# Performance work log

Hardware: AMD Instinct MI355X
Metric: run time of the kernel (lower is better)

The kernel has to match this reference:

```python
import jax, jax.numpy as jnp
import numpy as np

B, D, H, O, E = 16384, 1024, 512, 256, 8


def setup_inputs() -> dict:
    key = jax.random.key(0)
    ks = jax.random.split(key, 8)
    s = lambda k, shape, fan: (jax.random.normal(k, shape, jnp.float32) / np.sqrt(fan).astype(np.float32))
    z = lambda shape: jnp.zeros(shape, jnp.float32)
    return {
        "x": jax.random.normal(ks[0], (B, D), jnp.float32),
        # gating network: D -> 256 -> 128 -> E
        "gw1": s(ks[1], (D, 256), D), "gb1": z((256,)),
        "gw2": s(ks[2], (256, 128), 256), "gb2": z((128,)),
        "gw3": s(ks[3], (128, E), 128), "gb3": z((E,)),
        # experts, batched over expert dim E: D -> H -> H -> O
        "ew1": s(ks[4], (E, D, H), D), "eb1": z((E, H)),
        "ew2": s(ks[5], (E, H, H), H), "eb2": z((E, H)),
        "ew3": s(ks[6], (E, H, O), H), "eb3": z((E, O)),
    }


def reference(x, gw1, gb1, gw2, gb2, gw3, gb3, ew1, eb1, ew2, eb2, ew3, eb3):
    # Gating network (dropout is identity in eval mode)
    g = jax.nn.relu(x @ gw1 + gb1)
    g = jax.nn.relu(g @ gw2 + gb2)
    gates = jax.nn.softmax(g @ gw3 + gb3, axis=1)  # [B, E]
    # All experts run on every token: batched small MLPs over expert axis e
    h = jax.nn.relu(jnp.einsum('bd,edh->ebh', x, ew1) + eb1[:, None, :])   # [E, B, H]
    h = jax.nn.relu(jnp.einsum('ebh,ehk->ebk', h, ew2) + eb2[:, None, :])  # [E, B, H]
    eo = jnp.einsum('ebh,eho->ebo', h, ew3) + eb3[:, None, :]              # [E, B, O]
    # gate-weighted sum over experts
    out = jnp.einsum('ebo,be->bo', eo, gates)  # [B, O]
    return out
```

## Files before the change

kernel.cpp:

```cpp
#include <hip/hip_runtime.h>
#include <hip/hip_bf16.h>

typedef __hip_bfloat16 bf16;
typedef __attribute__((ext_vector_type(8))) __bf16 bf16x8;
typedef __attribute__((ext_vector_type(4))) float f32x4;

#define B_ 16384
#define D_ 1024
#define H_ 512
#define O_ 256
#define E_ 8
#define BC_ 8192
#define NG_ (E_ * H_ + 256)

static_assert(B_ % BC_ == 0, "chunking");

#define GLDS(src, dst) __builtin_amdgcn_global_load_lds( \
    (const __attribute__((address_space(1))) void*)(src), \
    (__attribute__((address_space(3))) void*)(dst), 16, 0, 0)

#define BAR()   asm volatile("s_barrier" ::: "memory")
#define LGKM0() do { asm volatile("s_waitcnt lgkmcnt(0)" ::: "memory"); \
                     __builtin_amdgcn_sched_barrier(0); } while (0)

__global__ void detect_k(const unsigned short* __restrict__ x, int* __restrict__ flag) {
    __shared__ int s;
    if (threadIdx.x == 0) s = 0;
    __syncthreads();
    int big = 0;
    for (int i = threadIdx.x; i < 2048; i += 256)
        if (((x[i] >> 7) & 0xFF) >= 150) big = 1;
    if (big) atomicOr(&s, 1);
    __syncthreads();
    if (threadIdx.x == 0) *flag = s;
}

__global__ void preproc_k(const void* x, bf16* xc,
                          const void* gb1, const void* gb2, const void* gw3,
                          const void* gb3, const void* eb1, const void* eb2,
                          const void* eb3,
                          bf16* gb1c, bf16* gb2c, bf16* gw3c, bf16* gb3c,
                          bf16* eb1c, bf16* eb2c, bf16* eb3c,
                          const void* gw1, const void* gw2,
                          const void* ew1, const void* ew2, const void* ew3,
                          bf16* gw1t, bf16* gw2t,
                          bf16* ew1t, bf16* ew2t, bf16* ew3t,
                          long ew3_zout, long ew3_cstride,
                          const int* __restrict__ flag) {
    const int f = *flag;
    const int tid = threadIdx.y * 32 + threadIdx.x;
    int lin = blockIdx.x;

    if (lin < 1024) {
        const long n8 = (long)B_ * D_ / 8;
        long i = (long)lin * 256 + tid;
        const long stride = 1024 * 256;
        if (f) {
            const float4* s = (const float4*)x;
            for (; i < n8; i += stride) {
                float4 a = s[2 * i], b = s[2 * i + 1];
                bf16 tmp[8];
                tmp[0] = __float2bfloat16(a.x); tmp[1] = __float2bfloat16(a.y);
                tmp[2] = __float2bfloat16(a.z); tmp[3] = __float2bfloat16(a.w);
                tmp[4] = __float2bfloat16(b.x); tmp[5] = __float2bfloat16(b.y);
                tmp[6] = __float2bfloat16(b.z); tmp[7] = __float2bfloat16(b.w);
                *(uint4*)(xc + i * 8) = *(const uint4*)tmp;
            }
        } else {
            const uint4* s = (const uint4*)x;
            for (; i < n8; i += stride) *(uint4*)(xc + i * 8) = s[i];
        }
        return;
    }
    if (lin < 1031) {
        const int id = lin - 1024;
        const void* sp[7] = {gb1, gb2, gw3, gb3, eb1, eb2, eb3};
        bf16* dp[7] = {gb1c, gb2c, gw3c, gb3c, eb1c, eb2c, eb3c};
        const int len[7] = {256, 128, 1024, 8, E_ * H_, E_ * H_, E_ * O_};
        const float* sf = (const float*)sp[id];
        const bf16*  sb = (const bf16*)sp[id];
        bf16* d = dp[id];
        for (int i = tid; i < len[id]; i += 256)
            d[i] = f ? __float2bfloat16(sf[i]) : sb[i];
        return;
    }
    lin -= 1031;
    __shared__ bf16 t[32][33];
    const void* src; bf16* dst; int R, C, bx, by, bz; long z_out, c_stride;
    if (lin < 256) {
        src = gw1; dst = gw1t; R = 1024; C = 256; z_out = 0; c_stride = 1024;
        bx = lin & 7; by = lin >> 3; bz = 0;
    } else if (lin < 288) {
        lin -= 256;
        src = gw2; dst = gw2t; R = 256; C = 128; z_out = 0; c_stride = 256;
        bx = lin & 3; by = lin >> 2; bz = 0;
    } else if (lin < 4384) {
        lin -= 288;
        src = ew1; dst = ew1t; R = 1024; C = 512;
        z_out = (long)H_ * D_; c_stride = D_;
        bx = lin & 15; by = (lin >> 4) & 31; bz = lin >> 9;
    } else if (lin < 6432) {
        lin -= 4384;
        src = ew2; dst = ew2t; R = 512; C = 512;
        z_out = (long)H_ * H_; c_stride = H_;
        bx = lin & 15; by = (lin >> 4) & 15; bz = lin >> 8;
    } else {
        lin -= 6432;
        src = ew3; dst = ew3t; R = 512; C = 256;
        z_out = ew3_zout; c_stride = ew3_cstride;
        bx = lin & 7; by = (lin >> 3) & 15; bz = lin >> 7;
    }
    const long zi = (long)bz * R * C;
    const int xg = bx * 32 + threadIdx.x;
    const int y0 = by * 32;
    const float* inf = (const float*)src;
    const bf16* inb = (const bf16*)src;
#pragma unroll
    for (int i = 0; i < 4; i++) {
        int r = y0 + threadIdx.y + i * 8;
        long idx = zi + (long)r * C + xg;
        t[threadIdx.y + i * 8][threadIdx.x] =
            f ? __float2bfloat16(inf[idx]) : inb[idx];
    }
    __syncthreads();
    const int xr = by * 32 + threadIdx.x;
    const long zo = (long)bz * z_out;
#pragma unroll
    for (int i = 0; i < 4; i++) {
        int c = bx * 32 + threadIdx.y + i * 8;
        dst[zo + (long)c * c_stride + xr] = t[threadIdx.x][threadIdx.y + i * 8];
    }
}

__global__ void gate3_softmax_k(const bf16* __restrict__ g2,
                                const bf16* __restrict__ gw3,
                                const bf16* __restrict__ gb3,
                                float* __restrict__ gates) {
    __shared__ float w[128 * 8];
    __shared__ float bsh[8];
    const int tid = threadIdx.x;
    for (int i = tid; i < 1024; i += 256) w[i] = __bfloat162float(gw3[i]);
    if (tid < 8) bsh[tid] = __bfloat162float(gb3[tid]);
    __syncthreads();

    const long row = (long)blockIdx.x * 256 + tid;
    float acc[8];
#pragma unroll
    for (int o = 0; o < 8; o++) acc[o] = bsh[o];

    const bf16x8* rp8 = (const bf16x8*)(g2 + row * 128);
#pragma unroll 4
    for (int c8 = 0; c8 < 16; c8++) {
        bf16x8 v8 = rp8[c8];
#pragma unroll
        for (int jj = 0; jj < 8; jj++) {
            float v = (float)v8[jj];
            int k = c8 * 8 + jj;
#pragma unroll
            for (int o = 0; o < 8; o++) acc[o] += v * w[k * 8 + o];
        }
    }
    float m = acc[0];
#pragma unroll
    for (int o = 1; o < 8; o++) m = fmaxf(m, acc[o]);
    float s = 0.f;
#pragma unroll
    for (int o = 0; o < 8; o++) { acc[o] = __expf(acc[o] - m); s += acc[o]; }
    const float inv = 1.f / s;
#pragma unroll
    for (int o = 0; o < 8; o++) gates[row * 8 + o] = acc[o] * inv;
}

template <int MODE>
__global__ __launch_bounds__(256, 4)
void gemm_bt(const bf16* __restrict__ A, const bf16* __restrict__ Bt,
             const bf16* __restrict__ bias, const float* __restrict__ gates,
             void* __restrict__ Cout, const bf16* __restrict__ eb3,
             int lda, int ldb, int ldo, int K,
             long a_z, long b_z, long bias_z, long out_z,
             int e_gate, int k_per_e, long a_e, long b_e, long row0) {
    __shared__ __attribute__((aligned(16))) bf16 As[128 * 32];
    __shared__ __attribute__((aligned(16))) bf16 Bs[128 * 32];

    const int tid  = threadIdx.x;
    const int lane = tid & 63;
    const int quad = lane >> 4;
    const int l15  = lane & 15;
    const int wid  = tid >> 6;
    const int wr   = (wid >> 1) << 6;
    const int wc   = (wid & 1) << 6;
    const int z    = blockIdx.z;
    const long m0  = (long)blockIdx.y << 7;
    const long n0  = (long)blockIdx.x << 7;

    const bf16* Az = A + (long)z * a_z;
    const bf16* Bz = Bt + (long)z * b_z;

    f32x4 acc[4][4];
#pragma unroll
    for (int i = 0; i < 4; i++)
#pragma unroll
        for (int j = 0; j < 4; j++) acc[i][j] = (f32x4){0.f, 0.f, 0.f, 0.f};

    const int erow = tid >> 2;
    const int ecol = (tid & 3) << 3;

    const int n_e   = k_per_e ? (K / k_per_e) : 1;
    const int inner = (k_per_e ? k_per_e : K) >> 5;

    for (int e = 0; e < n_e; e++) {
        const bf16* Ae = Az + (long)e * a_e;
        const bf16* Be = Bz + (long)e * b_e;
        for (int kti = 0; kti < inner; kti++) {
            const int kk = kti << 5;
#pragma unroll
            for (int i = 0; i < 2; i++) {
                const int r = (i << 6) + erow;
                GLDS(Ae + (m0 + r) * lda + (kk + ecol), As + r * 32 + ecol);
            }
#pragma unroll
            for (int i = 0; i < 2; i++) {
                const int r = (i << 6) + erow;
                GLDS(Be + (n0 + r) * ldb + (kk + ecol), Bs + r * 32 + ecol);
            }
            __syncthreads();
            bf16x8 af[4], bfr[4];
#pragma unroll
            for (int i = 0; i < 4; i++)
                af[i] = *(const bf16x8*)(As + (wr + i * 16 + l15) * 32 + (quad << 3));
#pragma unroll
            for (int j = 0; j < 4; j++)
                bfr[j] = *(const bf16x8*)(Bs + (wc + j * 16 + l15) * 32 + (quad << 3));
#pragma unroll
            for (int i = 0; i < 4; i++)
#pragma unroll
                for (int j = 0; j < 4; j++)
                    acc[i][j] = __builtin_amdgcn_mfma_f32_16x16x32_bf16(
                        af[i], bfr[j], acc[i][j], 0, 0, 0);
            __syncthreads();
        }
    }

    const int eg = (e_gate >= 0) ? e_gate : z;

    if constexpr (MODE == 0 || MODE == 1) {
        bf16* C = (bf16*)Cout + (long)z * out_z;
        const bf16* bb = bias + (long)z * bias_z;
        float gv[4][4];
        if constexpr (MODE == 1) {
#pragma unroll
            for (int i = 0; i < 4; i++)
#pragma unroll
                for (int rg = 0; rg < 4; rg++)
                    gv[i][rg] = gates[(row0 + m0 + wr + i * 16 + quad * 4 + rg) * 8 + eg];
        }
#pragma unroll
        for (int j = 0; j < 4; j++) {
            const int c = (int)n0 + wc + j * 16 + l15;
            const float bv = __bfloat162float(bb[c]);
#pragma unroll
            for (int i = 0; i < 4; i++) {
#pragma unroll
                for (int rg = 0; rg < 4; rg++) {
                    const long r = m0 + wr + i * 16 + quad * 4 + rg;
                    float v = fmaxf(acc[i][j][rg] + bv, 0.f);
                    if constexpr (MODE == 1) v *= gv[i][rg];
                    C[r * ldo + c] = __float2bfloat16(v);
                }
            }
        }
    } else if constexpr (MODE == 2) {
        float* C = (float*)Cout;
#pragma unroll
        for (int i = 0; i < 4; i++) {
#pragma unroll
            for (int rg = 0; rg < 4; rg++) {
                const long r = m0 + wr + i * 16 + quad * 4 + rg;
                const float g = gates[(row0 + r) * 8 + eg];
#pragma unroll
                for (int j = 0; j < 4; j++) {
                    const int c = (int)n0 + wc + j * 16 + l15;
                    const float b3 = __bfloat162float(eb3[eg * O_ + c]);
                    C[r * ldo + c] += acc[i][j][rg] + g * b3;
                }
            }
        }
    }
}

template <int MODE>
__global__ __launch_bounds__(512, 2)
void gemm256(const bf16* __restrict__ A, const bf16* __restrict__ Bt,
             const bf16* __restrict__ bias, const float* __restrict__ gates,
             void* __restrict__ Cout, const bf16* __restrict__ eb3,
             int lda, int ldb, int ldo, int K,
             long a_z, long b_z, long bias_z, long out_z, long row0) {
    __shared__ __attribute__((aligned(16))) bf16 lds[2][2][256 * 64];

    int bx = blockIdx.x, by = blockIdx.y;
    {
        const int gx = gridDim.x;
        const int nwg = gx * gridDim.y;
        if ((nwg & 7) == 0) {
            int lin = bx + gx * by;
            lin = (lin & 7) * (nwg >> 3) + (lin >> 3);
            bx = lin % gx; by = lin / gx;
        }
    }

    const int tid  = threadIdx.x;
    const int lane = tid & 63;
    const int quad = lane >> 4;
    const int l15  = lane & 15;
    const int w    = tid >> 6;
    const int wm   = w >> 2;
    const int wn   = w & 3;
    const int z    = blockIdx.z;
    const long m0  = (long)by << 8;
    const long n0  = (long)bx << 8;

    const bf16* __restrict__ Az = A + z * a_z;
    const bf16* __restrict__ Bz = Bt + z * b_z;

    f32x4 acc[8][4];
#pragma unroll
    for (int i = 0; i < 8; ++i)
#pragma unroll
        for (int j = 0; j < 4; ++j) acc[i][j] = (f32x4){0.f, 0.f, 0.f, 0.f};

    bf16x8 af[4][2], bv[2][2];

    auto stage = [&](int buf, int mat, int half, int kt) {
        const bf16* __restrict__ G = mat ? Bz : Az;
        const int ld = mat ? ldb : lda;
        const long p0 = mat ? n0 : m0;
#pragma unroll
        for (int l = 0; l < 2; ++l) {
            const int ci = (w << 1) | l;
            const int rb = mat ? ((ci >> 2) << 6) + (half << 5) + ((ci & 3) << 3)
                               : ((ci >> 3) << 7) + (half << 6) + ((ci & 7) << 3);
            const int row = rb + (lane >> 3);
            const int cb  = ((lane & 7) << 4) ^ ((row & 7) << 4);
            GLDS(G + (p0 + row) * ld + kt * 64 + (cb >> 1),
                 &lds[buf][mat][rb * 64]);
        }
    };
    auto ldaf = [&](int buf, int qm) {
#pragma unroll
        for (int i = 0; i < 4; ++i) {
            const int r = (wm << 7) + (qm << 6) + (i << 4) + l15;
            const char* p = (const char*)&lds[buf][0][r * 64];
            const int sw = (r & 7) << 4;
#pragma unroll
            for (int s = 0; s < 2; ++s)
                af[i][s] = *(const bf16x8*)(p + (((s << 6) + (quad << 4)) ^ sw));
        }
    };
    auto ldbf = [&](int buf, int qn) {
#pragma unroll
        for (int j = 0; j < 2; ++j) {
            const int r = (wn << 6) + (qn << 5) + (j << 4) + l15;
            const char* p = (const char*)&lds[buf][1][r * 64];
            const int sw = (r & 7) << 4;
#pragma unroll
            for (int s = 0; s < 2; ++s)
                bv[j][s] = *(const bf16x8*)(p + (((s << 6) + (quad << 4)) ^ sw));
        }
    };
    auto mmac = [&](int qm, int qn) {
#pragma unroll
        for (int i = 0; i < 4; ++i)
#pragma unroll
            for (int j = 0; j < 2; ++j)
#pragma unroll
                for (int s = 0; s < 2; ++s)
                    acc[(qm << 2) + i][(qn << 1) + j] =
                        __builtin_amdgcn_mfma_f32_16x16x32_bf16(
                            af[i][s], bv[j][s], acc[(qm << 2) + i][(qn << 1) + j],
                            0, 0, 0);
    };

    const int nt = K >> 6;

    stage(0, 0, 0, 0); stage(0, 0, 1, 0); stage(0, 1, 0, 0); stage(0, 1, 1, 0);
    stage(1, 0, 0, 1); stage(1, 1, 0, 1);
    asm volatile("s_waitcnt vmcnt(4)" ::: "memory");
    BAR();

    const int hi = nt >> 1;
    for (int it = 0; it < hi; ++it) {
        const int t1k = 2 * it + 1, t2k = 2 * it + 2, t3k = 2 * it + 3;
        const bool do2 = t2k < nt, do3 = t3k < nt;
        ldaf(0, 0); ldbf(0, 0); stage(1, 0, 1, t1k);
        BAR(); LGKM0();
        __builtin_amdgcn_s_setprio(1); mmac(0, 0); __builtin_amdgcn_s_setprio(0);
        BAR();
        ldbf(0, 1); stage(1, 1, 1, t1k);
        BAR(); LGKM0();
        __builtin_amdgcn_s_setprio(1); mmac(0, 1); __builtin_amdgcn_s_setprio(0);
        BAR();
        ldaf(0, 1); ldbf(0, 0); if (do2) stage(0, 0, 0, t2k);
        BAR(); LGKM0();
        __builtin_amdgcn_s_setprio(1); mmac(1, 0); __builtin_amdgcn_s_setprio(0);
        BAR();
        ldbf(0, 1); if (do2) stage(0, 1, 0, t2k);
        BAR(); LGKM0();
        __builtin_amdgcn_s_setprio(1); mmac(1, 1); __builtin_amdgcn_s_setprio(0);
        if (do2) { asm volatile("s_waitcnt vmcnt(4)" ::: "memory"); }
        else     { asm volatile("s_waitcnt vmcnt(0)" ::: "memory"); }
        BAR();
        ldaf(1, 0); ldbf(1, 0); if (do2) stage(0, 0, 1, t2k);
        BAR(); LGKM0();
        __builtin_amdgcn_s_setprio(1); mmac(0, 0); __builtin_amdgcn_s_setprio(0);
        BAR();
        ldbf(1, 1); if (do2) stage(0, 1, 1, t2k);
        BAR(); LGKM0();
        __builtin_amdgcn_s_setprio(1); mmac(0, 1); __builtin_amdgcn_s_setprio(0);
        BAR();
        ldaf(1, 1); ldbf(1, 0); if (do3) stage(1, 0, 0, t3k);
        BAR(); LGKM0();
        __builtin_amdgcn_s_setprio(1); mmac(1, 0); __builtin_amdgcn_s_setprio(0);
        BAR();
        ldbf(1, 1); if (do3) stage(1, 1, 0, t3k);
        BAR(); LGKM0();
        __builtin_amdgcn_s_setprio(1); mmac(1, 1); __builtin_amdgcn_s_setprio(0);
        if (do3) { asm volatile("s_waitcnt vmcnt(4)" ::: "memory"); }
        else     { asm volatile("s_waitcnt vmcnt(0)" ::: "memory"); }
        BAR();
    }

    if constexpr (MODE == 0 || MODE == 1) {
        bf16* C = (bf16*)Cout + z * out_z;
        const bf16* bb = bias + z * bias_z;
        float bvv[4];
#pragma unroll
        for (int jg = 0; jg < 4; ++jg)
            bvv[jg] = __bfloat162float(bb[(int)n0 + (wn << 6) + (jg << 4) + l15]);
#pragma unroll
        for (int ig = 0; ig < 8; ++ig) {
#pragma unroll
            for (int rg = 0; rg < 4; ++rg) {
                const long r = m0 + (wm << 7) + (ig << 4) + (quad << 2) + rg;
                float g = 1.f;
                if constexpr (MODE == 1) g = gates[(row0 + r) * 8 + z];
#pragma unroll
                for (int jg = 0; jg < 4; ++jg) {
                    const int c = (int)n0 + (wn << 6) + (jg << 4) + l15;
                    float v = fmaxf(acc[ig][jg][rg] + bvv[jg], 0.f);
                    if constexpr (MODE == 1) v *= g;
                    C[r * ldo + c] = __float2bfloat16(v);
                }
            }
        }
    } else if constexpr (MODE == 4) {
        float* C = (float*)Cout + z * out_z;
        float b3v[4];
#pragma unroll
        for (int jg = 0; jg < 4; ++jg)
            b3v[jg] = __bfloat162float(eb3[z * O_ + (int)n0 + (wn << 6) + (jg << 4) + l15]);
#pragma unroll
        for (int ig = 0; ig < 8; ++ig) {
#pragma unroll
            for (int rg = 0; rg < 4; ++rg) {
                const long r = m0 + (wm << 7) + (ig << 4) + (quad << 2) + rg;
                const float g = gates[(row0 + r) * 8 + z];
#pragma unroll
                for (int jg = 0; jg < 4; ++jg) {
                    const int c = (int)n0 + (wn << 6) + (jg << 4) + l15;
                    C[r * ldo + c] = acc[ig][jg][rg] + g * b3v[jg];
                }
            }
        }
    } else {
        float* C = (float*)Cout + z * out_z;
        const int e0 = z << 1;
        float b30[4], b31[4];
#pragma unroll
        for (int jg = 0; jg < 4; ++jg) {
            const int c = (int)n0 + (wn << 6) + (jg << 4) + l15;
            b30[jg] = __bfloat162float(eb3[e0 * O_ + c]);
            b31[jg] = __bfloat162float(eb3[(e0 + 1) * O_ + c]);
        }
#pragma unroll
        for (int ig = 0; ig < 8; ++ig) {
#pragma unroll
            for (int rg = 0; rg < 4; ++rg) {
                const long r = m0 + (wm << 7) + (ig << 4) + (quad << 2) + rg;
                const float g0 = gates[(row0 + r) * 8 + e0];
                const float g1 = gates[(row0 + r) * 8 + e0 + 1];
#pragma unroll
                for (int jg = 0; jg < 4; ++jg) {
                    const int c = (int)n0 + (wn << 6) + (jg << 4) + l15;
                    C[r * ldo + c] = acc[ig][jg][rg] + g0 * b30[jg] + g1 * b31[jg];
                }
            }
        }
    }
}

__global__ void zero_f32_k(float* __restrict__ p) {
    p[(long)blockIdx.x * 256 + threadIdx.x] = 0.f;
}
__global__ void out_cvt_k(const float* __restrict__ in, void* __restrict__ out,
                          const int* __restrict__ flag) {
    const long i = (long)blockIdx.x * 256 + threadIdx.x;
    if (*flag) ((float*)out)[i] = in[i];
    else       ((bf16*)out)[i] = __float2bfloat16(in[i]);
}
template <int NZ>
__global__ void reduceN_k(const float* __restrict__ p, void* __restrict__ out,
                          const int* __restrict__ flag, long n, long off) {
    const long i = ((long)blockIdx.x * 256 + threadIdx.x) * 4;
    float4 s = *(const float4*)(p + i);
#pragma unroll
    for (int zz = 1; zz < NZ; ++zz) {
        float4 a = *(const float4*)(p + (long)zz * n + i);
        s.x += a.x; s.y += a.y; s.z += a.z; s.w += a.w;
    }
    if (*flag) {
        *(float4*)((float*)out + off + i) = s;
    } else {
        bf16* o = (bf16*)out + off + i;
        o[0] = __float2bfloat16(s.x); o[1] = __float2bfloat16(s.y);
        o[2] = __float2bfloat16(s.z); o[3] = __float2bfloat16(s.w);
    }
}

extern "C" void kernel_launch(void* const* d_in, const int* in_sizes, int n_in,
                              void* d_out, int out_size, void* d_ws, size_t ws_size,
                              hipStream_t stream) {
    (void)in_sizes; (void)n_in; (void)out_size;
    const void* x   = d_in[0];
    const void* gw1 = d_in[1];
    const void* gb1 = d_in[2];
    const void* gw2 = d_in[3];
    const void* gb2 = d_in[4];
    const void* gw3 = d_in[5];
    const void* gb3 = d_in[6];
    const void* ew1 = d_in[7];
    const void* eb1 = d_in[8];
    const void* ew2 = d_in[9];
    const void* eb2 = d_in[10];
    const void* ew3 = d_in[11];
    const void* eb3 = d_in[12];

    char* ws = (char*)d_ws;
    size_t off = 0;
    auto alloc = [&](size_t n) { char* p = ws + off; off += (n + 255) & ~(size_t)255; return p; };

    int*  flag  = (int*)alloc(256);
    bf16* xc    = (bf16*)alloc((size_t)B_ * D_ * 2);
    bf16* ew1g  = (bf16*)alloc((size_t)NG_ * D_ * 2);
    bf16* ew1t  = ew1g;
    bf16* gw1t  = ew1g + (size_t)E_ * H_ * D_;
    bf16* gw2t  = (bf16*)alloc((size_t)128 * 256 * 2);
    bf16* ew2t  = (bf16*)alloc((size_t)E_ * H_ * H_ * 2);
    bf16* ew3t  = (bf16*)alloc((size_t)E_ * O_ * H_ * 2);
    bf16* eb1g  = (bf16*)alloc((size_t)NG_ * 2);
    bf16* eb1c  = eb1g;
    bf16* gb1c  = eb1g + E_ * H_;
    bf16* gb2c  = (bf16*)alloc(128 * 2);
    bf16* gw3c  = (bf16*)alloc(1024 * 2);
    bf16* gb3c  = (bf16*)alloc(8 * 2);
    bf16* eb2c  = (bf16*)alloc((size_t)E_ * H_ * 2);
    bf16* eb3c  = (bf16*)alloc((size_t)E_ * O_ * 2);
    bf16* g2b   = (bf16*)alloc((size_t)B_ * 128 * 2);
    float* gates = (float*)alloc((size_t)B_ * 8 * 4);

    const size_t smallCore = off;
    const size_t needFused = smallCore + ((size_t)BC_ * NG_ * 2 + 256)
                                       + ((size_t)B_ * E_ * H_ * 2 + 256) + 4096;
    const size_t g1sz = (size_t)B_ * 256 * 2 + 256;
    const size_t needChunk = smallCore + g1sz + ((size_t)E_ * BC_ * H_ * 2 + 256)
                                       + ((size_t)BC_ * E_ * H_ * 2 + 256)
                                       + (8ull * BC_ * O_ * 4 + 256) + 4096;
    const bool pathFused = ws_size >= needFused;
    const bool pathChunk = ws_size >= needChunk;

    detect_k<<<1, 256, 0, stream>>>((const unsigned short*)x, flag);

    const bool l3pair = pathFused || pathChunk;
    const long e3zo = l3pair ? (long)H_ : (long)O_ * H_;
    const long e3cs = l3pair ? (long)E_ * H_ : (long)H_;
    preproc_k<<<8487, dim3(32, 8), 0, stream>>>(
        x, xc, gb1, gb2, gw3, gb3, eb1, eb2, eb3,
        gb1c, gb2c, gw3c, gb3c, eb1c, eb2c, eb3c,
        gw1, gw2, ew1, ew2, ew3, gw1t, gw2t, ew1t, ew2t, ew3t,
        e3zo, e3cs, flag);

    if (pathFused) {
        bf16* h1gc = (bf16*)alloc((size_t)BC_ * NG_ * 2);
        bf16* h2   = (bf16*)alloc((size_t)B_ * E_ * H_ * 2);
        float* parts = (float*)h1gc;

        for (int ch = 0; ch < B_ / BC_; ch++) {
            const long rb = (long)ch * BC_;
            gemm256<0><<<dim3(NG_ / 256, BC_ / 256, 1), 512, 0, stream>>>(
                xc + rb * D_, ew1g, eb1g, nullptr, h1gc, nullptr,
                D_, D_, NG_, D_,
                0, 0, 0, 0, 0);
            gemm_bt<0><<<dim3(1, BC_ / 128, 1), 256, 0, stream>>>(
                h1gc + (size_t)E_ * H_, gw2t, gb2c, nullptr,
                g2b + rb * 128, nullptr,
                NG_, 256, 128, 256, 0, 0, 0, 0, 0, 0, 0, 0, 0);
            gate3_softmax_k<<<dim3(BC_ / 256), 256, 0, stream>>>(
                g2b + rb * 128, gw3c, gb3c, gates + rb * 8);
            gemm256<1><<<dim3(2, BC_ / 256, 8), 512, 0, stream>>>(
                h1gc, ew2t, eb2c, gates, h2 + rb * (long)E_ * H_, nullptr,
                NG_, H_, E_ * H_, H_,
                (long)H_, (long)H_ * H_, (long)H_, (long)H_, rb);
        }
        gemm256<5><<<dim3(1, B_ / 256, 4), 512, 0, stream>>>(
            h2, ew3t, nullptr, gates, parts, eb3c,
            E_ * H_, E_ * H_, O_, 1024,
            2L * H_, 2L * H_, 0, (long)B_ * O_, 0);
        reduceN_k<4><<<dim3(B_ * O_ / 1024), 256, 0, stream>>>(
            parts, d_out, flag, (long)B_ * O_, 0L);
        return;
    }

    bf16* g1 = (bf16*)alloc((size_t)B_ * 256 * 2);
    gemm_bt<0><<<dim3(2, 128, 1), 256, 0, stream>>>(
        xc, gw1t, gb1c, nullptr, g1, nullptr,
        1024, 1024, 256, 1024, 0, 0, 0, 0, 0, 0, 0, 0, 0);
    gemm_bt<0><<<dim3(1, 128, 1), 256, 0, stream>>>(
        g1, gw2t, gb2c, nullptr, g2b, nullptr,
        256, 256, 128, 256, 0, 0, 0, 0, 0, 0, 0, 0, 0);
    gate3_softmax_k<<<dim3(B_ / 256), 256, 0, stream>>>(g2b, gw3c, gb3c, gates);

    if (pathChunk) {
        bf16* h1c = (bf16*)alloc((size_t)E_ * BC_ * H_ * 2);
        bf16* h2c = (bf16*)alloc((size_t)BC_ * E_ * H_ * 2);
        float* parts = (float*)alloc(8ull * BC_ * O_ * 4);

        for (int ch = 0; ch < B_ / BC_; ch++) {
            const long rb = (long)ch * BC_;
            gemm256<0><<<dim3(2, BC_ / 256, 8), 512, 0, stream>>>(
                xc + rb * D_, ew1t, eb1c, nullptr, h1c, nullptr,
                D_, D_, H_, D_,
                0, (long)H_ * D_, (long)H_, (long)BC_ * H_, 0);
            gemm256<1><<<dim3(2, BC_ / 256, 8), 512, 0, stream>>>(
                h1c, ew2t, eb2c, gates, h2c, nullptr,
                H_, H_, E_ * H_, H_,
                (long)BC_ * H_, (long)H_ * H_, (long)H_, (long)H_, rb);
            gemm256<4><<<dim3(1, BC_ / 256, 8), 512, 0, stream>>>(
                h2c, ew3t, nullptr, gates, parts, eb3c,
                E_ * H_, E_ * H_, O_, 512,
                (long)H_, (long)H_, 0, (long)BC_ * O_, rb);
            reduceN_k<8><<<dim3(BC_ * O_ / 1024), 256, 0, stream>>>(
                parts, d_out, flag, (long)BC_ * O_, rb * O_);
        }
    } else {
        bf16* h1s = (bf16*)alloc((size_t)B_ * H_ * 2);
        bf16* h2s = (bf16*)alloc((size_t)B_ * H_ * 2);
        float* oacc = (float*)alloc((size_t)B_ * O_ * 4);
        zero_f32_k<<<dim3(B_ * O_ / 256), 256, 0, stream>>>(oacc);
        for (int e = 0; e < E_; e++) {
            gemm_bt<0><<<dim3(4, 128, 1), 256, 0, stream>>>(
                xc, ew1t + (size_t)e * H_ * D_, eb1c + (size_t)e * H_, nullptr, h1s, nullptr,
                1024, 1024, 512, 1024, 0, 0, 0, 0, 0, 0, 0, 0, 0);
            gemm_bt<1><<<dim3(4, 128, 1), 256, 0, stream>>>(
                h1s, ew2t + (size_t)e * H_ * H_, eb2c + (size_t)e * H_, gates, h2s, nullptr,
                512, 512, 512, 512, 0, 0, 0, 0, e, 0, 0, 0, 0);
            gemm_bt<2><<<dim3(2, 128, 1), 256, 0, stream>>>(
                h2s, ew3t + (size_t)e * O_ * H_, nullptr, gates, oacc, eb3c,
                512, 512, 256, 512, 0, 0, 0, 0, e, 0, 0, 0, 0);
        }
        out_cvt_k<<<dim3(B_ * O_ / 256), 256, 0, stream>>>(oacc, d_out, flag);
    }
}
```

Before: 542.3 us.

## Split gating layer-1 out of fused expert GEMM into separate gating pass

Removes the path that concatenated the gating first-layer weights onto the expert layer-1 weights, which computed both in one wide GEMM per chunk. The gating network now runs up front on the full batch via separate small GEMMs and softmax. Each chunk then runs a batched per-expert layer-1 GEMM followed by the gated layer-2 GEMM, and a paired layer-3 GEMM plus reduce finishes the output. This trades the fused wide launch for an expert-batched launch layout and restores separate gating kernels.

```diff
diff --git a/kernel.cpp b/kernel.cpp
--- a/kernel.cpp
+++ b/kernel.cpp
@@ -11,7 +11,6 @@
 #define O_ 256
 #define E_ 8
 #define BC_ 8192
-#define NG_ (E_ * H_ + 256)
 
 static_assert(B_ % BC_ == 0, "chunking");
 
@@ -550,15 +549,13 @@
 
     int*  flag  = (int*)alloc(256);
     bf16* xc    = (bf16*)alloc((size_t)B_ * D_ * 2);
-    bf16* ew1g  = (bf16*)alloc((size_t)NG_ * D_ * 2);
-    bf16* ew1t  = ew1g;
-    bf16* gw1t  = ew1g + (size_t)E_ * H_ * D_;
+    bf16* ew1t  = (bf16*)alloc((size_t)E_ * H_ * D_ * 2);
+    bf16* gw1t  = (bf16*)alloc((size_t)256 * 1024 * 2);
     bf16* gw2t  = (bf16*)alloc((size_t)128 * 256 * 2);
     bf16* ew2t  = (bf16*)alloc((size_t)E_ * H_ * H_ * 2);
     bf16* ew3t  = (bf16*)alloc((size_t)E_ * O_ * H_ * 2);
-    bf16* eb1g  = (bf16*)alloc((size_t)NG_ * 2);
-    bf16* eb1c  = eb1g;
-    bf16* gb1c  = eb1g + E_ * H_;
+    bf16* eb1c  = (bf16*)alloc((size_t)E_ * H_ * 2);
+    bf16* gb1c  = (bf16*)alloc(256 * 2);
     bf16* gb2c  = (bf16*)alloc(128 * 2);
     bf16* gw3c  = (bf16*)alloc(1024 * 2);
     bf16* gb3c  = (bf16*)alloc(8 * 2);
@@ -566,20 +563,20 @@
     bf16* eb3c  = (bf16*)alloc((size_t)E_ * O_ * 2);
     bf16* g2b   = (bf16*)alloc((size_t)B_ * 128 * 2);
     float* gates = (float*)alloc((size_t)B_ * 8 * 4);
+    bf16* g1    = (bf16*)alloc((size_t)B_ * 256 * 2);
 
     const size_t smallCore = off;
-    const size_t needFused = smallCore + ((size_t)BC_ * NG_ * 2 + 256)
-                                       + ((size_t)B_ * E_ * H_ * 2 + 256) + 4096;
-    const size_t g1sz = (size_t)B_ * 256 * 2 + 256;
-    const size_t needChunk = smallCore + g1sz + ((size_t)E_ * BC_ * H_ * 2 + 256)
+    const size_t needPair = smallCore + ((size_t)E_ * BC_ * H_ * 2 + 256)
+                                      + ((size_t)B_ * E_ * H_ * 2 + 256) + 4096;
+    const size_t needChunk = smallCore + ((size_t)E_ * BC_ * H_ * 2 + 256)
                                        + ((size_t)BC_ * E_ * H_ * 2 + 256)
                                        + (8ull * BC_ * O_ * 4 + 256) + 4096;
-    const bool pathFused = ws_size >= needFused;
+    const bool pathPair  = ws_size >= needPair;
     const bool pathChunk = ws_size >= needChunk;
 
     detect_k<<<1, 256, 0, stream>>>((const unsigned short*)x, flag);
 
-    const bool l3pair = pathFused || pathChunk;
+    const bool l3pair = pathPair || pathChunk;
     const long e3zo = l3pair ? (long)H_ : (long)O_ * H_;
     const long e3cs = l3pair ? (long)E_ * H_ : (long)H_;
     preproc_k<<<8487, dim3(32, 8), 0, stream>>>(
@@ -588,38 +585,6 @@
         gw1, gw2, ew1, ew2, ew3, gw1t, gw2t, ew1t, ew2t, ew3t,
         e3zo, e3cs, flag);
 
-    if (pathFused) {
-        bf16* h1gc = (bf16*)alloc((size_t)BC_ * NG_ * 2);
-        bf16* h2   = (bf16*)alloc((size_t)B_ * E_ * H_ * 2);
-        float* parts = (float*)h1gc;
-
-        for (int ch = 0; ch < B_ / BC_; ch++) {
-            const long rb = (long)ch * BC_;
-            gemm256<0><<<dim3(NG_ / 256, BC_ / 256, 1), 512, 0, stream>>>(
-                xc + rb * D_, ew1g, eb1g, nullptr, h1gc, nullptr,
-                D_, D_, NG_, D_,
-                0, 0, 0, 0, 0);
-            gemm_bt<0><<<dim3(1, BC_ / 128, 1), 256, 0, stream>>>(
-                h1gc + (size_t)E_ * H_, gw2t, gb2c, nullptr,
-                g2b + rb * 128, nullptr,
-                NG_, 256, 128, 256, 0, 0, 0, 0, 0, 0, 0, 0, 0);
-            gate3_softmax_k<<<dim3(BC_ / 256), 256, 0, stream>>>(
-                g2b + rb * 128, gw3c, gb3c, gates + rb * 8);
-            gemm256<1><<<dim3(2, BC_ / 256, 8), 512, 0, stream>>>(
-                h1gc, ew2t, eb2c, gates, h2 + rb * (long)E_ * H_, nullptr,
-                NG_, H_, E_ * H_, H_,
-                (long)H_, (long)H_ * H_, (long)H_, (long)H_, rb);
-        }
-        gemm256<5><<<dim3(1, B_ / 256, 4), 512, 0, stream>>>(
-            h2, ew3t, nullptr, gates, parts, eb3c,
-            E_ * H_, E_ * H_, O_, 1024,
-            2L * H_, 2L * H_, 0, (long)B_ * O_, 0);
-        reduceN_k<4><<<dim3(B_ * O_ / 1024), 256, 0, stream>>>(
-            parts, d_out, flag, (long)B_ * O_, 0L);
-        return;
-    }
-
-    bf16* g1 = (bf16*)alloc((size_t)B_ * 256 * 2);
     gemm_bt<0><<<dim3(2, 128, 1), 256, 0, stream>>>(
         xc, gw1t, gb1c, nullptr, g1, nullptr,
         1024, 1024, 256, 1024, 0, 0, 0, 0, 0, 0, 0, 0, 0);
@@ -628,7 +593,29 @@
         256, 256, 128, 256, 0, 0, 0, 0, 0, 0, 0, 0, 0);
     gate3_softmax_k<<<dim3(B_ / 256), 256, 0, stream>>>(g2b, gw3c, gb3c, gates);
 
-    if (pathChunk) {
+    if (pathPair) {
+        bf16* h1c = (bf16*)alloc((size_t)E_ * BC_ * H_ * 2);
+        bf16* h2  = (bf16*)alloc((size_t)B_ * E_ * H_ * 2);
+        float* parts = (float*)h1c;
+
+        for (int ch = 0; ch < B_ / BC_; ch++) {
+            const long rb = (long)ch * BC_;
+            gemm256<0><<<dim3(2, BC_ / 256, 8), 512, 0, stream>>>(
+                xc + rb * D_, ew1t, eb1c, nullptr, h1c, nullptr,
+                D_, D_, H_, D_,
+                0, (long)H_ * D_, (long)H_, (long)BC_ * H_, 0);
+            gemm256<1><<<dim3(2, BC_ / 256, 8), 512, 0, stream>>>(
+                h1c, ew2t, eb2c, gates, h2 + rb * (long)E_ * H_, nullptr,
+                H_, H_, E_ * H_, H_,
+                (long)BC_ * H_, (long)H_ * H_, (long)H_, (long)H_, rb);
+        }
+        gemm256<5><<<dim3(1, B_ / 256, 4), 512, 0, stream>>>(
+            h2, ew3t, nullptr, gates, parts, eb3c,
+            E_ * H_, E_ * H_, O_, 1024,
+            2L * H_, 2L * H_, 0, (long)B_ * O_, 0);
+        reduceN_k<4><<<dim3(B_ * O_ / 1024), 256, 0, stream>>>(
+            parts, d_out, flag, (long)B_ * O_, 0L);
+    } else if (pathChunk) {
         bf16* h1c = (bf16*)alloc((size_t)E_ * BC_ * H_ * 2);
         bf16* h2c = (bf16*)alloc((size_t)BC_ * E_ * H_ * 2);
         float* parts = (float*)alloc(8ull * BC_ * O_ * 4);
```

Result: faster. 494.9 us (-8.8%).
